# Kernel optimization log

Measured on AMD Instinct MI355X. Metric: run time of the kernel, lower is better.

## Reference

```python
import jax, jax.numpy as jnp
import numpy as np

D = 512          # feature dim
N = 4095         # context length
LMBD = 0.9       # eligibility-trace decay
DIM = 2 * D + 1  # 1025
CTX = N + 1      # 4096


def make_M(n: int, lmbd: float) -> jnp.ndarray:
    # M[row, col] = lmbd**(row-col) for col <= row < n, col < n; last row and
    # last column are all zero (M[-1, -1] explicitly zeroed in the original).
    i = jnp.arange(n, dtype=jnp.int32)
    diff = i[:, None] - i[None, :]
    core = jnp.where(diff >= 0, jnp.float32(lmbd) ** jnp.maximum(diff, 0).astype(jnp.float32), 0.0)
    M = jnp.zeros((n + 1, n + 1), dtype=jnp.float32)
    return M.at[:n, :n].set(core)


def setup_inputs() -> dict:
    key = jax.random.key(0)
    kz, kp, kq = jax.random.split(key, 3)
    Z = jax.random.normal(kz, (DIM, CTX), dtype=jnp.float32)
    # nn.Parameter(torch.empty(...)) is uninitialized in the source; use small
    # random values as stand-ins for trained parameters.
    P = jax.random.normal(kp, (DIM, DIM), dtype=jnp.float32) * 0.02
    Q = jax.random.normal(kq, (DIM, DIM), dtype=jnp.float32) * 0.02
    M = make_M(N, LMBD)
    return {"Z": Z, "P": P, "Q": Q, "M": M}


def reference(Z, P, Q, M):
    # X = Z^T Q Z : (CTX, CTX) bilinear attention scores
    X = jnp.einsum("dn,de,em->nm", Z, Q, Z)
    A = jax.nn.softmax(X, axis=-1)          # activation
    # Z + (1/n) * P @ Z @ M @ A ; contract left-to-right to keep (DIM, CTX) intermediates
    PZ = P @ Z                               # (DIM, CTX)
    PZM = PZ @ M                             # (DIM, CTX), M lower-tri decay
    return Z + (1.0 / N) * (PZM @ A)
```

## Files before the change

kernel.cpp:

```cpp
#include <hip/hip_runtime.h>


#define LMBD 0.9f
#define CTXN 4096
#define DIMN 1025
#define DP 1152

#define KSPLIT 1024
#define PSTRIDE ((size_t)DP * CTXN)

typedef __bf16 bf16x8 __attribute__((ext_vector_type(8)));
typedef float f32x4 __attribute__((ext_vector_type(4)));
typedef long lx2 __attribute__((ext_vector_type(2)));

__device__ __forceinline__ unsigned short f2bf(float f) {
  union { float f; unsigned u; } v; v.f = f;
  unsigned r = v.u + 0x7FFFu + ((v.u >> 16) & 1u);
  return (unsigned short)(r >> 16);
}
__device__ __forceinline__ float bf2f(unsigned short h) {
  union { unsigned u; float f; } v; v.u = ((unsigned)h) << 16;
  return v.f;
}

__device__ __forceinline__ void gld_lds16(const void* g, void* l) {
  __builtin_amdgcn_global_load_lds(
      (const __attribute__((address_space(1))) unsigned int*)g,
      (__attribute__((address_space(3))) unsigned int*)l, 16, 0, 0);
}

template <int MODE, int TM, int TN>
__device__ __forceinline__ void gemm_body(
    const unsigned short* __restrict__ A, const unsigned short* __restrict__ B,
    void* __restrict__ Cout, int K, int lda, int ldb, int ldc, int bi, int bj,
    float* __restrict__ pmax, float* __restrict__ psum) {
  constexpr int FI = TM / 32, FJ = TN / 32;
  __shared__ unsigned short sA[TM * 64];
  __shared__ unsigned short sB[TN * 64];
  const int tid = threadIdx.x;
  const int wave = tid >> 6;
  const int lane = tid & 63;
  const long i0 = (long)bi * TM;
  const long j0 = (long)bj * TN;
  const int wm = (wave & 1) * (TM / 2);
  const int wn = (wave >> 1) * (TN / 2);

  f32x4 acc[FI][FJ] = {};

  const int srow8 = lane >> 3;
  const int gk = ((lane & 7) - srow8) & 7;
  const int mrow = lane & 15;
  const int q2 = lane >> 4;

  for (int k0 = 0; k0 < K; k0 += 64) {
    __syncthreads();
#pragma unroll
    for (int c = 0; c < TM / 32; ++c) {
      const int q = wave * (TM / 32) + c;
      gld_lds16(A + (i0 + q * 8 + srow8) * (long)lda + k0 + gk * 8, &sA[q * 512]);
    }
#pragma unroll
    for (int c = 0; c < TN / 32; ++c) {
      const int q = wave * (TN / 32) + c;
      gld_lds16(B + (j0 + q * 8 + srow8) * (long)ldb + k0 + gk * 8, &sB[q * 512]);
    }
    __syncthreads();
#pragma unroll
    for (int kk = 0; kk < 2; ++kk) {
      const int slot = ((kk * 4 + q2) + mrow) & 7;
      bf16x8 af[FI], bfr[FJ];
#pragma unroll
      for (int i = 0; i < FI; ++i)
        af[i] = *(const bf16x8*)&sA[(wm + i * 16 + mrow) * 64 + slot * 8];
#pragma unroll
      for (int j = 0; j < FJ; ++j)
        bfr[j] = *(const bf16x8*)&sB[(wn + j * 16 + mrow) * 64 + slot * 8];
#pragma unroll
      for (int i = 0; i < FI; ++i)
#pragma unroll
        for (int j = 0; j < FJ; ++j)
          acc[i][j] =
              __builtin_amdgcn_mfma_f32_16x16x32_bf16(af[i], bfr[j], acc[i][j], 0, 0, 0);
    }
  }

  const int lr = (lane >> 4) * 4;
  const int lc = lane & 15;
#pragma unroll
  for (int i = 0; i < FI; ++i) {
#pragma unroll
    for (int j = 0; j < FJ; ++j) {
#pragma unroll
      for (int r = 0; r < 4; ++r) {
        const long row = i0 + wm + i * 16 + lr + r;
        const long col = j0 + wn + j * 16 + lc;
        const float v = acc[i][j][r];
        if (MODE == 1) ((float*)Cout)[row * ldc + col] = v;
        else ((unsigned short*)Cout)[row * ldc + col] = f2bf(v);
      }
    }
  }

  if constexpr (MODE == 4) {
    float* sMax = (float*)sA;
    float* sSum = (float*)sB;
    const int k8 = (wave & 1) * 4 + (lane >> 4);
    __syncthreads();
#pragma unroll
    for (int j = 0; j < FJ; ++j) {
      float m = -1e30f;
#pragma unroll
      for (int i = 0; i < FI; ++i)
#pragma unroll
        for (int r = 0; r < 4; ++r) m = fmaxf(m, acc[i][j][r]);
      float sv = 0.f;
#pragma unroll
      for (int i = 0; i < FI; ++i)
#pragma unroll
        for (int r = 0; r < 4; ++r) sv += __expf(acc[i][j][r] - m);
      const int c = wn + j * 16 + lc;
      sMax[c * 8 + k8] = m;
      sSum[c * 8 + k8] = sv;
    }
    __syncthreads();
    if (tid < 128) {
      float m = -1e30f;
#pragma unroll
      for (int k = 0; k < 8; ++k) m = fmaxf(m, sMax[tid * 8 + k]);
      float sv = 0.f;
#pragma unroll
      for (int k = 0; k < 8; ++k) sv += sSum[tid * 8 + k] * __expf(sMax[tid * 8 + k] - m);
      pmax[(size_t)bi * CTXN + j0 + tid] = m;
      psum[(size_t)bi * CTXN + j0 + tid] = sv;
    }
  }
}

__global__ __launch_bounds__(256, 2) void gemm_xt(
    const unsigned short* __restrict__ QZT, const unsigned short* __restrict__ ZbT,
    unsigned short* __restrict__ XT, float* __restrict__ pmax,
    float* __restrict__ psum) {
  gemm_body<4, 128, 128>(QZT, ZbT, XT, DP, DP, DP, CTXN, blockIdx.x, blockIdx.y, pmax,
                         psum);
}

__global__ __launch_bounds__(256, 2) void gemm_dual(
    const unsigned short* __restrict__ ZbT, const unsigned short* __restrict__ Qb,
    unsigned short* __restrict__ QZT, const unsigned short* __restrict__ Pb,
    float* __restrict__ PZ) {
  const unsigned g = blockIdx.x;
  if (g < 576) {
    gemm_body<0, 128, 64>(ZbT, Qb, QZT, DP, DP, DP, DP, g & 31, g >> 5, nullptr,
                          nullptr);
  } else {
    const unsigned h = g - 576;
    gemm_body<1, 64, 128>(Pb, ZbT, PZ, DP, DP, DP, CTXN, h >> 5, h & 31, nullptr,
                          nullptr);
  }
}

__global__ __launch_bounds__(256, 2) void gemm_fp8_splitk(
    const unsigned char* __restrict__ A, const unsigned char* __restrict__ B,
    unsigned short* __restrict__ Cout) {
  __shared__ unsigned char sA[128 * 64];
  __shared__ unsigned char sB[128 * 64];
  const int tid = threadIdx.x;
  const int wave = tid >> 6;
  const int lane = tid & 63;
  const unsigned g = blockIdx.x;
  const unsigned bj = g & 31;
  const unsigned t = g >> 5;
  const unsigned bi = t >> 2;
  const unsigned bz = t & 3;
  const long i0 = (long)bi * 128;
  const long j0 = (long)bj * 128;
  const int wm = (wave & 1) * 64;
  const int wn = (wave >> 1) * 64;
  const int kb = bz * KSPLIT;
  Cout += (size_t)bz * PSTRIDE;

  f32x4 acc[4][4] = {};
  const int srow = lane >> 2;
  const int skc = (((lane & 3) - (lane >> 3)) & 3) * 16;
  const int mrow = lane & 15;
  const int slot = ((((lane >> 4) + (mrow >> 1)) & 3)) * 16;

  for (int k0 = kb; k0 < kb + KSPLIT; k0 += 64) {
    __syncthreads();
#pragma unroll
    for (int c = 0; c < 2; ++c) {
      const int q = wave * 2 + c;
      gld_lds16(A + (i0 + q * 16 + srow) * (long)CTXN + k0 + skc, &sA[q * 1024]);
      gld_lds16(B + (j0 + q * 16 + srow) * (long)CTXN + k0 + skc, &sB[q * 1024]);
    }
    __syncthreads();
    lx2 af[4], bfr[4];
#pragma unroll
    for (int i = 0; i < 4; ++i)
      af[i] = *(const lx2*)&sA[(wm + i * 16 + mrow) * 64 + slot];
#pragma unroll
    for (int j = 0; j < 4; ++j)
      bfr[j] = *(const lx2*)&sB[(wn + j * 16 + mrow) * 64 + slot];
#pragma unroll
    for (int i = 0; i < 4; ++i)
#pragma unroll
      for (int j = 0; j < 4; ++j) {
        acc[i][j] = __builtin_amdgcn_mfma_f32_16x16x32_fp8_fp8(af[i].x, bfr[j].x,
                                                               acc[i][j], 0, 0, 0);
        acc[i][j] = __builtin_amdgcn_mfma_f32_16x16x32_fp8_fp8(af[i].y, bfr[j].y,
                                                               acc[i][j], 0, 0, 0);
      }
  }

  const int lr = (lane >> 4) * 4;
  const int lc = lane & 15;
#pragma unroll
  for (int i = 0; i < 4; ++i)
#pragma unroll
    for (int j = 0; j < 4; ++j)
#pragma unroll
      for (int r = 0; r < 4; ++r) {
        const long row = i0 + wm + i * 16 + lr + r;
        if (row < DIMN)
          Cout[row * (long)CTXN + j0 + wn + j * 16 + lc] = f2bf(acc[i][j][r]);
      }
}

__global__ void reduce_kernel(const unsigned short* __restrict__ Pt,
                              const float* __restrict__ Z, float* __restrict__ out) {
  const size_t idx = ((size_t)blockIdx.x * 256 + threadIdx.x) * 4;
  float ax = 0.f, ay = 0.f, az = 0.f, aw = 0.f;
#pragma unroll
  for (int z = 0; z < 4; ++z) {
    const ushort4 v = *(const ushort4*)&Pt[(size_t)z * PSTRIDE + idx];
    ax += bf2f(v.x); ay += bf2f(v.y); az += bf2f(v.z); aw += bf2f(v.w);
  }
  const f32x4 zv = *(const f32x4*)&Z[idx];
  f32x4 o;
  o[0] = zv[0] + ax * 0.00390625f;
  o[1] = zv[1] + ay * 0.00390625f;
  o[2] = zv[2] + az * 0.00390625f;
  o[3] = zv[3] + aw * 0.00390625f;
  *(f32x4*)&out[idx] = o;
}

__global__ void prep_kernel(const float* __restrict__ Z, const float* __restrict__ Q,
                            const float* __restrict__ P,
                            unsigned short* __restrict__ ZbT,
                            unsigned short* __restrict__ Qb,
                            unsigned short* __restrict__ Pb) {
  __shared__ float tile[32][33];
  const unsigned g = blockIdx.x;
  const int tid = threadIdx.x;
  if (g < 4608) {
    const int n0 = (g & 127) * 32, e0 = (g >> 7) * 32;
    const int tx = tid & 31, ty = tid >> 5;
#pragma unroll
    for (int k = 0; k < 4; ++k) {
      const int e = e0 + ty + k * 8;
      tile[ty + k * 8][tx] = (e < DIMN) ? Z[(size_t)e * CTXN + n0 + tx] : 0.f;
    }
    __syncthreads();
#pragma unroll
    for (int k = 0; k < 4; ++k) {
      const int n = n0 + ty + k * 8;
      ZbT[(size_t)n * DP + e0 + tx] = f2bf(tile[tx][ty + k * 8]);
    }
  } else {
    const unsigned id2 = g - 4608;
    const int mat = id2 >= 1296;
    const float* src = mat ? P : Q;
    unsigned short* dst = mat ? Pb : Qb;
    const unsigned e0 = (id2 - (mat ? 1296u : 0u)) * 1024u + tid * 4u;
    const unsigned r = e0 / 1152u;
    const unsigned c = e0 - r * 1152u;
    ushort4 o;
    o.x = (r < DIMN && c + 0 < DIMN) ? f2bf(src[(size_t)r * DIMN + c + 0]) : 0;
    o.y = (r < DIMN && c + 1 < DIMN) ? f2bf(src[(size_t)r * DIMN + c + 1]) : 0;
    o.z = (r < DIMN && c + 2 < DIMN) ? f2bf(src[(size_t)r * DIMN + c + 2]) : 0;
    o.w = (r < DIMN && c + 3 < DIMN) ? f2bf(src[(size_t)r * DIMN + c + 3]) : 0;
    *(ushort4*)&dst[(size_t)r * DP + c] = o;
  }
}

__global__ void red2_kernel(const float* __restrict__ pmax, const float* __restrict__ psum,
                            float* __restrict__ rowmax, float* __restrict__ inv_l) {
  const int n = blockIdx.x * 256 + threadIdx.x;
  float M = -1e30f;
  for (int c = 0; c < 32; ++c) M = fmaxf(M, pmax[(size_t)c * CTXN + n]);
  float s = 0.f;
  for (int c = 0; c < 32; ++c)
    s += psum[(size_t)c * CTXN + n] * __expf(pmax[(size_t)c * CTXN + n] - M);
  rowmax[n] = M;
  inv_l[n] = 1.0f / (4095.0f * s);
}

__global__ __launch_bounds__(256) void ewscan_kernel(
    const unsigned short* __restrict__ XT, const float* __restrict__ rowmax,
    unsigned int* __restrict__ ET, const float* __restrict__ PZ,
    const float* __restrict__ inv_l, unsigned char* __restrict__ PZMb) {
  __shared__ float sF[256];
  const unsigned g = blockIdx.x;
  const int t = threadIdx.x;
  if (g >= 1152) {
    const size_t idx = ((size_t)(g - 1152) * 256 + t) * 4;
    const ushort4 v = *(const ushort4*)&XT[idx];
    const int n = (int)(idx & 4095);
    const float4 rm = *(const float4*)&rowmax[n];
    unsigned p = __builtin_amdgcn_cvt_pk_fp8_f32(__expf(bf2f(v.x) - rm.x),
                                                 __expf(bf2f(v.y) - rm.y), 0, false);
    p = __builtin_amdgcn_cvt_pk_fp8_f32(__expf(bf2f(v.z) - rm.z),
                                        __expf(bf2f(v.w) - rm.w), p, true);
    ET[idx >> 2] = p;
    return;
  }
  const int d = g;
  const float* row = PZ + (size_t)d * CTXN;
  float x[16];
#pragma unroll
  for (int q = 0; q < 4; ++q) {
    const float4 v = *(const float4*)&row[t * 16 + q * 4];
    x[q * 4 + 0] = v.x; x[q * 4 + 1] = v.y; x[q * 4 + 2] = v.z; x[q * 4 + 3] = v.w;
  }
  if (t == 255) x[15] = 0.f;
  float loc[16];
  float run = 0.f;
#pragma unroll
  for (int i = 15; i >= 0; --i) { run = run * LMBD + x[i]; loc[i] = run; }
  float f = loc[0];
  sF[t] = f;
  __syncthreads();
  float mlt = 0.1853020188851841f;
  for (int step = 1; step < 256; step <<= 1) {
    const float other = (t + step < 256) ? sF[t + step] : 0.f;
    __syncthreads();
    f += mlt * other;
    mlt *= mlt;
    sF[t] = f;
    __syncthreads();
  }
  const float R = (t < 255) ? sF[t + 1] : 0.f;
  float il[16];
#pragma unroll
  for (int q = 0; q < 4; ++q) {
    const float4 v = *(const float4*)&inv_l[t * 16 + q * 4];
    il[q * 4 + 0] = v.x * 256.f; il[q * 4 + 1] = v.y * 256.f;
    il[q * 4 + 2] = v.z * 256.f; il[q * 4 + 3] = v.w * 256.f;
  }
  float o[16];
  float p = 1.f;
#pragma unroll
  for (int i = 15; i >= 0; --i) {
    p *= LMBD;
    o[i] = (loc[i] + p * R) * il[i];
  }
  unsigned w[4];
#pragma unroll
  for (int q = 0; q < 4; ++q) {
    unsigned pk = __builtin_amdgcn_cvt_pk_fp8_f32(o[q * 4 + 0], o[q * 4 + 1], 0, false);
    pk = __builtin_amdgcn_cvt_pk_fp8_f32(o[q * 4 + 2], o[q * 4 + 3], pk, true);
    w[q] = pk;
  }
  *(uint4*)&PZMb[(size_t)d * CTXN + t * 16] = make_uint4(w[0], w[1], w[2], w[3]);
}

extern "C" void kernel_launch(void* const* d_in, const int* in_sizes, int n_in,
                              void* d_out, int out_size, void* d_ws, size_t ws_size,
                              hipStream_t stream) {
  const float* Z = (const float*)d_in[0];
  const float* P = (const float*)d_in[1];
  const float* Q = (const float*)d_in[2];

  char* ws = (char*)d_ws;
  size_t off = 0;
  auto alloc = [&](size_t bytes) {
    void* p = ws + off;
    off += (bytes + 255) & ~(size_t)255;
    return p;
  };
  unsigned char* ET   = (unsigned char*)alloc((size_t)CTXN * CTXN);
  unsigned char* PZMb = (unsigned char*)alloc((size_t)DP * CTXN);
  float* rowmax       = (float*)alloc((size_t)CTXN * 4);
  float* inv_l        = (float*)alloc((size_t)CTXN * 4);
  char* pool = (char*)alloc(0);
  unsigned short* ZbT = (unsigned short*)alloc((size_t)CTXN * DP * 2);
  unsigned short* QZT = (unsigned short*)alloc((size_t)CTXN * DP * 2);
  unsigned short* XT  = (unsigned short*)alloc((size_t)CTXN * CTXN * 2);
  float* PZ           = (float*)alloc((size_t)DP * CTXN * 4);
  unsigned short* Qb  = (unsigned short*)alloc((size_t)DP * DP * 2);
  unsigned short* Pb  = (unsigned short*)alloc((size_t)DP * DP * 2);
  float* pmax         = (float*)alloc((size_t)32 * CTXN * 4);
  float* psum         = (float*)alloc((size_t)32 * CTXN * 4);
  unsigned short* partials = (unsigned short*)pool;
  if (off > ws_size) return;

  prep_kernel<<<7200, 256, 0, stream>>>(Z, Q, P, ZbT, Qb, Pb);

  gemm_dual<<<1152, 256, 0, stream>>>(ZbT, Qb, QZT, Pb, PZ);

  gemm_xt<<<dim3(32, 32), 256, 0, stream>>>(QZT, ZbT, XT, pmax, psum);

  red2_kernel<<<16, 256, 0, stream>>>(pmax, psum, rowmax, inv_l);

  ewscan_kernel<<<17536, 256, 0, stream>>>(XT, rowmax, (unsigned int*)ET, PZ, inv_l,
                                           PZMb);

  gemm_fp8_splitk<<<1152, 256, 0, stream>>>(PZMb, ET, partials);
  reduce_kernel<<<4100, 256, 0, stream>>>(partials, Z, (float*)d_out);
}
```

Measured before the change: 248.6 us.

## Fuse all stages into one cooperative persistent kernel with grid syncs

Replaces the seven separate kernel launches with a single cooperative kernel of 512 persistent blocks that loops over each stage's work units and separates stages with grid-wide syncs. Shared memory becomes one fixed 32KB buffer reused by every stage. The goal is to remove per-launch overhead and the tail gaps between kernels. In exchange, every stage runs at a fixed grid size and at the occupancy of the largest shared-memory user, and grid.sync adds its own cost. If the cooperative launch fails, the code falls back to the separate kernels.

```diff
diff --git a/kernel.cpp b/kernel.cpp
--- a/kernel.cpp
+++ b/kernel.cpp
@@ -1,4 +1,7 @@
 #include <hip/hip_runtime.h>
+#include <hip/hip_cooperative_groups.h>
+
+namespace cg = cooperative_groups;
 
 
 #define LMBD 0.9f
@@ -13,6 +16,15 @@
 typedef float f32x4 __attribute__((ext_vector_type(4)));
 typedef long lx2 __attribute__((ext_vector_type(2)));
 
+struct KParams {
+  const float *Z, *P, *Q;
+  unsigned short *ZbT, *QZT, *XT, *Qb, *Pb;
+  float *PZ, *pmax, *psum, *rowmax, *inv_l;
+  unsigned char *ET, *PZMb;
+  unsigned short *partials;
+  float *out;
+};
+
 __device__ __forceinline__ unsigned short f2bf(float f) {
   union { float f; unsigned u; } v; v.f = f;
   unsigned r = v.u + 0x7FFFu + ((v.u >> 16) & 1u);
@@ -31,12 +43,13 @@
 
 template <int MODE, int TM, int TN>
 __device__ __forceinline__ void gemm_body(
-    const unsigned short* __restrict__ A, const unsigned short* __restrict__ B,
-    void* __restrict__ Cout, int K, int lda, int ldb, int ldc, int bi, int bj,
-    float* __restrict__ pmax, float* __restrict__ psum) {
+    char* smem, const unsigned short* __restrict__ A,
+    const unsigned short* __restrict__ B, void* __restrict__ Cout, int K, int lda,
+    int ldb, int ldc, int bi, int bj, float* __restrict__ pmax,
+    float* __restrict__ psum) {
   constexpr int FI = TM / 32, FJ = TN / 32;
-  __shared__ unsigned short sA[TM * 64];
-  __shared__ unsigned short sB[TN * 64];
+  unsigned short* sA = (unsigned short*)smem;
+  unsigned short* sB = sA + TM * 64;
   const int tid = threadIdx.x;
   const int wave = tid >> 6;
   const int lane = tid & 63;
@@ -136,38 +149,140 @@
   }
 }
 
-__global__ __launch_bounds__(256, 2) void gemm_xt(
-    const unsigned short* __restrict__ QZT, const unsigned short* __restrict__ ZbT,
-    unsigned short* __restrict__ XT, float* __restrict__ pmax,
-    float* __restrict__ psum) {
-  gemm_body<4, 128, 128>(QZT, ZbT, XT, DP, DP, DP, CTXN, blockIdx.x, blockIdx.y, pmax,
-                         psum);
-}
-
-__global__ __launch_bounds__(256, 2) void gemm_dual(
-    const unsigned short* __restrict__ ZbT, const unsigned short* __restrict__ Qb,
-    unsigned short* __restrict__ QZT, const unsigned short* __restrict__ Pb,
-    float* __restrict__ PZ) {
-  const unsigned g = blockIdx.x;
+
+__device__ __forceinline__ void prep_unit(char* smem, unsigned g, const KParams& a) {
+  float* tile = (float*)smem;
+  const int tid = threadIdx.x;
+  if (g < 4608) {
+    const int n0 = (g & 127) * 32, e0 = (g >> 7) * 32;
+    const int tx = tid & 31, ty = tid >> 5;
+    __syncthreads();
+#pragma unroll
+    for (int k = 0; k < 4; ++k) {
+      const int e = e0 + ty + k * 8;
+      tile[(ty + k * 8) * 33 + tx] = (e < DIMN) ? a.Z[(size_t)e * CTXN + n0 + tx] : 0.f;
+    }
+    __syncthreads();
+#pragma unroll
+    for (int k = 0; k < 4; ++k) {
+      const int n = n0 + ty + k * 8;
+      a.ZbT[(size_t)n * DP + e0 + tx] = f2bf(tile[tx * 33 + ty + k * 8]);
+    }
+  } else {
+    const unsigned id2 = g - 4608;
+    const int mat = id2 >= 1296;
+    const float* src = mat ? a.P : a.Q;
+    unsigned short* dst = mat ? a.Pb : a.Qb;
+    const unsigned e0 = (id2 - (mat ? 1296u : 0u)) * 1024u + tid * 4u;
+    const unsigned r = e0 / 1152u;
+    const unsigned c = e0 - r * 1152u;
+    ushort4 o;
+    o.x = (r < DIMN && c + 0 < DIMN) ? f2bf(src[(size_t)r * DIMN + c + 0]) : 0;
+    o.y = (r < DIMN && c + 1 < DIMN) ? f2bf(src[(size_t)r * DIMN + c + 1]) : 0;
+    o.z = (r < DIMN && c + 2 < DIMN) ? f2bf(src[(size_t)r * DIMN + c + 2]) : 0;
+    o.w = (r < DIMN && c + 3 < DIMN) ? f2bf(src[(size_t)r * DIMN + c + 3]) : 0;
+    *(ushort4*)&dst[(size_t)r * DP + c] = o;
+  }
+}
+
+__device__ __forceinline__ void dual_unit(char* smem, unsigned g, const KParams& a) {
   if (g < 576) {
-    gemm_body<0, 128, 64>(ZbT, Qb, QZT, DP, DP, DP, DP, g & 31, g >> 5, nullptr,
-                          nullptr);
+    gemm_body<0, 128, 64>(smem, a.ZbT, a.Qb, a.QZT, DP, DP, DP, DP, g & 31, g >> 5,
+                          nullptr, nullptr);
   } else {
     const unsigned h = g - 576;
-    gemm_body<1, 64, 128>(Pb, ZbT, PZ, DP, DP, DP, CTXN, h >> 5, h & 31, nullptr,
-                          nullptr);
-  }
-}
-
-__global__ __launch_bounds__(256, 2) void gemm_fp8_splitk(
-    const unsigned char* __restrict__ A, const unsigned char* __restrict__ B,
-    unsigned short* __restrict__ Cout) {
-  __shared__ unsigned char sA[128 * 64];
-  __shared__ unsigned char sB[128 * 64];
+    gemm_body<1, 64, 128>(smem, a.Pb, a.ZbT, a.PZ, DP, DP, DP, CTXN, h >> 5, h & 31,
+                          nullptr, nullptr);
+  }
+}
+
+__device__ __forceinline__ void xt_unit(char* smem, unsigned u, const KParams& a) {
+  gemm_body<4, 128, 128>(smem, a.QZT, a.ZbT, a.XT, DP, DP, DP, CTXN, u & 31, u >> 5,
+                         a.pmax, a.psum);
+}
+
+__device__ __forceinline__ void red2_unit(unsigned u, const KParams& a) {
+  const int n = (int)u * 256 + threadIdx.x;
+  float M = -1e30f;
+  for (int c = 0; c < 32; ++c) M = fmaxf(M, a.pmax[(size_t)c * CTXN + n]);
+  float s = 0.f;
+  for (int c = 0; c < 32; ++c)
+    s += a.psum[(size_t)c * CTXN + n] * __expf(a.pmax[(size_t)c * CTXN + n] - M);
+  a.rowmax[n] = M;
+  a.inv_l[n] = 1.0f / (4095.0f * s);
+}
+
+__device__ __forceinline__ void ewscan_unit(float* sF, unsigned g, const KParams& a) {
+  const int t = threadIdx.x;
+  if (g >= 1152) {
+    const size_t idx = ((size_t)(g - 1152) * 256 + t) * 4;
+    const ushort4 v = *(const ushort4*)&a.XT[idx];
+    const int n = (int)(idx & 4095);
+    const float4 rm = *(const float4*)&a.rowmax[n];
+    unsigned p = __builtin_amdgcn_cvt_pk_fp8_f32(__expf(bf2f(v.x) - rm.x),
+                                                 __expf(bf2f(v.y) - rm.y), 0, false);
+    p = __builtin_amdgcn_cvt_pk_fp8_f32(__expf(bf2f(v.z) - rm.z),
+                                        __expf(bf2f(v.w) - rm.w), p, true);
+    ((unsigned int*)a.ET)[idx >> 2] = p;
+    return;
+  }
+  const int d = (int)g;
+  const float* row = a.PZ + (size_t)d * CTXN;
+  float x[16];
+#pragma unroll
+  for (int q = 0; q < 4; ++q) {
+    const float4 v = *(const float4*)&row[t * 16 + q * 4];
+    x[q * 4 + 0] = v.x; x[q * 4 + 1] = v.y; x[q * 4 + 2] = v.z; x[q * 4 + 3] = v.w;
+  }
+  if (t == 255) x[15] = 0.f;
+  float loc[16];
+  float run = 0.f;
+#pragma unroll
+  for (int i = 15; i >= 0; --i) { run = run * LMBD + x[i]; loc[i] = run; }
+  __syncthreads();
+  float f = loc[0];
+  sF[t] = f;
+  __syncthreads();
+  float mlt = 0.1853020188851841f;
+  for (int step = 1; step < 256; step <<= 1) {
+    const float other = (t + step < 256) ? sF[t + step] : 0.f;
+    __syncthreads();
+    f += mlt * other;
+    mlt *= mlt;
+    sF[t] = f;
+    __syncthreads();
+  }
+  const float R = (t < 255) ? sF[t + 1] : 0.f;
+  float il[16];
+#pragma unroll
+  for (int q = 0; q < 4; ++q) {
+    const float4 v = *(const float4*)&a.inv_l[t * 16 + q * 4];
+    il[q * 4 + 0] = v.x * 256.f; il[q * 4 + 1] = v.y * 256.f;
+    il[q * 4 + 2] = v.z * 256.f; il[q * 4 + 3] = v.w * 256.f;
+  }
+  float o[16];
+  float p = 1.f;
+#pragma unroll
+  for (int i = 15; i >= 0; --i) {
+    p *= LMBD;
+    o[i] = (loc[i] + p * R) * il[i];
+  }
+  unsigned w[4];
+#pragma unroll
+  for (int q = 0; q < 4; ++q) {
+    unsigned pk = __builtin_amdgcn_cvt_pk_fp8_f32(o[q * 4 + 0], o[q * 4 + 1], 0, false);
+    pk = __builtin_amdgcn_cvt_pk_fp8_f32(o[q * 4 + 2], o[q * 4 + 3], pk, true);
+    w[q] = pk;
+  }
+  *(uint4*)&a.PZMb[(size_t)d * CTXN + t * 16] = make_uint4(w[0], w[1], w[2], w[3]);
+}
+
+__device__ __forceinline__ void fp8_unit(char* smem, unsigned g, const KParams& a) {
+  unsigned char* sA = (unsigned char*)smem;
+  unsigned char* sB = sA + 128 * 64;
   const int tid = threadIdx.x;
   const int wave = tid >> 6;
   const int lane = tid & 63;
-  const unsigned g = blockIdx.x;
   const unsigned bj = g & 31;
   const unsigned t = g >> 5;
   const unsigned bi = t >> 2;
@@ -177,7 +292,7 @@
   const int wm = (wave & 1) * 64;
   const int wn = (wave >> 1) * 64;
   const int kb = bz * KSPLIT;
-  Cout += (size_t)bz * PSTRIDE;
+  unsigned short* Cout = a.partials + (size_t)bz * PSTRIDE;
 
   f32x4 acc[4][4] = {};
   const int srow = lane >> 2;
@@ -190,8 +305,8 @@
 #pragma unroll
     for (int c = 0; c < 2; ++c) {
       const int q = wave * 2 + c;
-      gld_lds16(A + (i0 + q * 16 + srow) * (long)CTXN + k0 + skc, &sA[q * 1024]);
-      gld_lds16(B + (j0 + q * 16 + srow) * (long)CTXN + k0 + skc, &sB[q * 1024]);
+      gld_lds16(a.PZMb + (i0 + q * 16 + srow) * (long)CTXN + k0 + skc, &sA[q * 1024]);
+      gld_lds16(a.ET + (j0 + q * 16 + srow) * (long)CTXN + k0 + skc, &sB[q * 1024]);
     }
     __syncthreads();
     lx2 af[4], bfr[4];
@@ -226,150 +341,74 @@
       }
 }
 
-__global__ void reduce_kernel(const unsigned short* __restrict__ Pt,
-                              const float* __restrict__ Z, float* __restrict__ out) {
-  const size_t idx = ((size_t)blockIdx.x * 256 + threadIdx.x) * 4;
+__device__ __forceinline__ void reduce_unit(unsigned u, const KParams& a) {
+  const size_t idx = ((size_t)u * 256 + threadIdx.x) * 4;
   float ax = 0.f, ay = 0.f, az = 0.f, aw = 0.f;
 #pragma unroll
   for (int z = 0; z < 4; ++z) {
-    const ushort4 v = *(const ushort4*)&Pt[(size_t)z * PSTRIDE + idx];
+    const ushort4 v = *(const ushort4*)&a.partials[(size_t)z * PSTRIDE + idx];
     ax += bf2f(v.x); ay += bf2f(v.y); az += bf2f(v.z); aw += bf2f(v.w);
   }
-  const f32x4 zv = *(const f32x4*)&Z[idx];
+  const f32x4 zv = *(const f32x4*)&a.Z[idx];
   f32x4 o;
   o[0] = zv[0] + ax * 0.00390625f;
   o[1] = zv[1] + ay * 0.00390625f;
   o[2] = zv[2] + az * 0.00390625f;
   o[3] = zv[3] + aw * 0.00390625f;
-  *(f32x4*)&out[idx] = o;
-}
-
-__global__ void prep_kernel(const float* __restrict__ Z, const float* __restrict__ Q,
-                            const float* __restrict__ P,
-                            unsigned short* __restrict__ ZbT,
-                            unsigned short* __restrict__ Qb,
-                            unsigned short* __restrict__ Pb) {
-  __shared__ float tile[32][33];
-  const unsigned g = blockIdx.x;
-  const int tid = threadIdx.x;
-  if (g < 4608) {
-    const int n0 = (g & 127) * 32, e0 = (g >> 7) * 32;
-    const int tx = tid & 31, ty = tid >> 5;
-#pragma unroll
-    for (int k = 0; k < 4; ++k) {
-      const int e = e0 + ty + k * 8;
-      tile[ty + k * 8][tx] = (e < DIMN) ? Z[(size_t)e * CTXN + n0 + tx] : 0.f;
-    }
-    __syncthreads();
-#pragma unroll
-    for (int k = 0; k < 4; ++k) {
-      const int n = n0 + ty + k * 8;
-      ZbT[(size_t)n * DP + e0 + tx] = f2bf(tile[tx][ty + k * 8]);
-    }
-  } else {
-    const unsigned id2 = g - 4608;
-    const int mat = id2 >= 1296;
-    const float* src = mat ? P : Q;
-    unsigned short* dst = mat ? Pb : Qb;
-    const unsigned e0 = (id2 - (mat ? 1296u : 0u)) * 1024u + tid * 4u;
-    const unsigned r = e0 / 1152u;
-    const unsigned c = e0 - r * 1152u;
-    ushort4 o;
-    o.x = (r < DIMN && c + 0 < DIMN) ? f2bf(src[(size_t)r * DIMN + c + 0]) : 0;
-    o.y = (r < DIMN && c + 1 < DIMN) ? f2bf(src[(size_t)r * DIMN + c + 1]) : 0;
-    o.z = (r < DIMN && c + 2 < DIMN) ? f2bf(src[(size_t)r * DIMN + c + 2]) : 0;
-    o.w = (r < DIMN && c + 3 < DIMN) ? f2bf(src[(size_t)r * DIMN + c + 3]) : 0;
-    *(ushort4*)&dst[(size_t)r * DP + c] = o;
-  }
-}
-
-__global__ void red2_kernel(const float* __restrict__ pmax, const float* __restrict__ psum,
-                            float* __restrict__ rowmax, float* __restrict__ inv_l) {
-  const int n = blockIdx.x * 256 + threadIdx.x;
-  float M = -1e30f;
-  for (int c = 0; c < 32; ++c) M = fmaxf(M, pmax[(size_t)c * CTXN + n]);
-  float s = 0.f;
-  for (int c = 0; c < 32; ++c)
-    s += psum[(size_t)c * CTXN + n] * __expf(pmax[(size_t)c * CTXN + n] - M);
-  rowmax[n] = M;
-  inv_l[n] = 1.0f / (4095.0f * s);
-}
-
-__global__ __launch_bounds__(256) void ewscan_kernel(
-    const unsigned short* __restrict__ XT, const float* __restrict__ rowmax,
-    unsigned int* __restrict__ ET, const float* __restrict__ PZ,
-    const float* __restrict__ inv_l, unsigned char* __restrict__ PZMb) {
+  *(f32x4*)&a.out[idx] = o;
+}
+
+__global__ __launch_bounds__(256, 2) void mega(KParams a) {
+  __shared__ __align__(16) char smem[32768];
+  cg::grid_group grid = cg::this_grid();
+  const unsigned nb = gridDim.x;
+  const unsigned b0 = blockIdx.x;
+
+  for (unsigned u = b0; u < 7200; u += nb) prep_unit(smem, u, a);
+  grid.sync();
+  for (unsigned u = b0; u < 1152; u += nb) dual_unit(smem, u, a);
+  grid.sync();
+  for (unsigned u = b0; u < 1024; u += nb) xt_unit(smem, u, a);
+  grid.sync();
+  for (unsigned u = b0; u < 16; u += nb) red2_unit(u, a);
+  grid.sync();
+  for (unsigned u = b0; u < 17536; u += nb) ewscan_unit((float*)smem, u, a);
+  grid.sync();
+  for (unsigned u = b0; u < 1152; u += nb) fp8_unit(smem, u, a);
+  grid.sync();
+  for (unsigned u = b0; u < 4100; u += nb) reduce_unit(u, a);
+}
+
+__global__ void prep_k(KParams a) {
+  __shared__ __align__(16) char smem[4352];
+  prep_unit(smem, blockIdx.x, a);
+}
+__global__ __launch_bounds__(256, 2) void dual_k(KParams a) {
+  __shared__ __align__(16) char smem[24576];
+  dual_unit(smem, blockIdx.x, a);
+}
+__global__ __launch_bounds__(256, 2) void xt_k(KParams a) {
+  __shared__ __align__(16) char smem[32768];
+  xt_unit(smem, blockIdx.x, a);
+}
+__global__ void red2_k(KParams a) { red2_unit(blockIdx.x, a); }
+__global__ __launch_bounds__(256) void ewscan_k(KParams a) {
   __shared__ float sF[256];
-  const unsigned g = blockIdx.x;
-  const int t = threadIdx.x;
-  if (g >= 1152) {
-    const size_t idx = ((size_t)(g - 1152) * 256 + t) * 4;
-    const ushort4 v = *(const ushort4*)&XT[idx];
-    const int n = (int)(idx & 4095);
-    const float4 rm = *(const float4*)&rowmax[n];
-    unsigned p = __builtin_amdgcn_cvt_pk_fp8_f32(__expf(bf2f(v.x) - rm.x),
-                                                 __expf(bf2f(v.y) - rm.y), 0, false);
-    p = __builtin_amdgcn_cvt_pk_fp8_f32(__expf(bf2f(v.z) - rm.z),
-                                        __expf(bf2f(v.w) - rm.w), p, true);
-    ET[idx >> 2] = p;
-    return;
-  }
-  const int d = g;
-  const float* row = PZ + (size_t)d * CTXN;
-  float x[16];
-#pragma unroll
-  for (int q = 0; q < 4; ++q) {
-    const float4 v = *(const float4*)&row[t * 16 + q * 4];
-    x[q * 4 + 0] = v.x; x[q * 4 + 1] = v.y; x[q * 4 + 2] = v.z; x[q * 4 + 3] = v.w;
-  }
-  if (t == 255) x[15] = 0.f;
-  float loc[16];
-  float run = 0.f;
-#pragma unroll
-  for (int i = 15; i >= 0; --i) { run = run * LMBD + x[i]; loc[i] = run; }
-  float f = loc[0];
-  sF[t] = f;
-  __syncthreads();
-  float mlt = 0.1853020188851841f;
-  for (int step = 1; step < 256; step <<= 1) {
-    const float other = (t + step < 256) ? sF[t + step] : 0.f;
-    __syncthreads();
-    f += mlt * other;
-    mlt *= mlt;
-    sF[t] = f;
-    __syncthreads();
-  }
-  const float R = (t < 255) ? sF[t + 1] : 0.f;
-  float il[16];
-#pragma unroll
-  for (int q = 0; q < 4; ++q) {
-    const float4 v = *(const float4*)&inv_l[t * 16 + q * 4];
-    il[q * 4 + 0] = v.x * 256.f; il[q * 4 + 1] = v.y * 256.f;
-    il[q * 4 + 2] = v.z * 256.f; il[q * 4 + 3] = v.w * 256.f;
-  }
-  float o[16];
-  float p = 1.f;
-#pragma unroll
-  for (int i = 15; i >= 0; --i) {
-    p *= LMBD;
-    o[i] = (loc[i] + p * R) * il[i];
-  }
-  unsigned w[4];
-#pragma unroll
-  for (int q = 0; q < 4; ++q) {
-    unsigned pk = __builtin_amdgcn_cvt_pk_fp8_f32(o[q * 4 + 0], o[q * 4 + 1], 0, false);
-    pk = __builtin_amdgcn_cvt_pk_fp8_f32(o[q * 4 + 2], o[q * 4 + 3], pk, true);
-    w[q] = pk;
-  }
-  *(uint4*)&PZMb[(size_t)d * CTXN + t * 16] = make_uint4(w[0], w[1], w[2], w[3]);
-}
+  ewscan_unit(sF, blockIdx.x, a);
+}
+__global__ __launch_bounds__(256, 2) void fp8_k(KParams a) {
+  __shared__ __align__(16) char smem[16384];
+  fp8_unit(smem, blockIdx.x, a);
+}
+__global__ void reduce_k(KParams a) { reduce_unit(blockIdx.x, a); }
 
 extern "C" void kernel_launch(void* const* d_in, const int* in_sizes, int n_in,
                               void* d_out, int out_size, void* d_ws, size_t ws_size,
                               hipStream_t stream) {
-  const float* Z = (const float*)d_in[0];
-  const float* P = (const float*)d_in[1];
-  const float* Q = (const float*)d_in[2];
+  KParams a;
+  a.Z = (const float*)d_in[0];
+  a.P = (const float*)d_in[1];
+  a.Q = (const float*)d_in[2];
 
   char* ws = (char*)d_ws;
   size_t off = 0;
@@ -378,33 +417,34 @@
     off += (bytes + 255) & ~(size_t)255;
     return p;
   };
-  unsigned char* ET   = (unsigned char*)alloc((size_t)CTXN * CTXN);
-  unsigned char* PZMb = (unsigned char*)alloc((size_t)DP * CTXN);
-  float* rowmax       = (float*)alloc((size_t)CTXN * 4);
-  float* inv_l        = (float*)alloc((size_t)CTXN * 4);
+  a.ET     = (unsigned char*)alloc((size_t)CTXN * CTXN);
+  a.PZMb   = (unsigned char*)alloc((size_t)DP * CTXN);
+  a.rowmax = (float*)alloc((size_t)CTXN * 4);
+  a.inv_l  = (float*)alloc((size_t)CTXN * 4);
   char* pool = (char*)alloc(0);
-  unsigned short* ZbT = (unsigned short*)alloc((size_t)CTXN * DP * 2);
-  unsigned short* QZT = (unsigned short*)alloc((size_t)CTXN * DP * 2);
-  unsigned short* XT  = (unsigned short*)alloc((size_t)CTXN * CTXN * 2);
-  float* PZ           = (float*)alloc((size_t)DP * CTXN * 4);
-  unsigned short* Qb  = (unsigned short*)alloc((size_t)DP * DP * 2);
-  unsigned short* Pb  = (unsigned short*)alloc((size_t)DP * DP * 2);
-  float* pmax         = (float*)alloc((size_t)32 * CTXN * 4);
-  float* psum         = (float*)alloc((size_t)32 * CTXN * 4);
-  unsigned short* partials = (unsigned short*)pool;
+  a.ZbT  = (unsigned short*)alloc((size_t)CTXN * DP * 2);
+  a.QZT  = (unsigned short*)alloc((size_t)CTXN * DP * 2);
+  a.XT   = (unsigned short*)alloc((size_t)CTXN * CTXN * 2);
+  a.PZ   = (float*)alloc((size_t)DP * CTXN * 4);
+  a.Qb   = (unsigned short*)alloc((size_t)DP * DP * 2);
+  a.Pb   = (unsigned short*)alloc((size_t)DP * DP * 2);
+  a.pmax = (float*)alloc((size_t)32 * CTXN * 4);
+  a.psum = (float*)alloc((size_t)32 * CTXN * 4);
+  a.partials = (unsigned short*)pool;
+  a.out = (float*)d_out;
   if (off > ws_size) return;
 
-  prep_kernel<<<7200, 256, 0, stream>>>(Z, Q, P, ZbT, Qb, Pb);
-
-  gemm_dual<<<1152, 256, 0, stream>>>(ZbT, Qb, QZT, Pb, PZ);
-
-  gemm_xt<<<dim3(32, 32), 256, 0, stream>>>(QZT, ZbT, XT, pmax, psum);
-
-  red2_kernel<<<16, 256, 0, stream>>>(pmax, psum, rowmax, inv_l);
-
-  ewscan_kernel<<<17536, 256, 0, stream>>>(XT, rowmax, (unsigned int*)ET, PZ, inv_l,
-                                           PZMb);
-
-  gemm_fp8_splitk<<<1152, 256, 0, stream>>>(PZMb, ET, partials);
-  reduce_kernel<<<4100, 256, 0, stream>>>(partials, Z, (float*)d_out);
-}
+  void* kargs[] = {(void*)&a};
+  hipError_t err =
+      hipLaunchCooperativeKernel(mega, dim3(512), dim3(256), kargs, 0u, stream);
+  if (err != hipSuccess) {
+    (void)hipGetLastError();
+    prep_k<<<7200, 256, 0, stream>>>(a);
+    dual_k<<<1152, 256, 0, stream>>>(a);
+    xt_k<<<1024, 256, 0, stream>>>(a);
+    red2_k<<<16, 256, 0, stream>>>(a);
+    ewscan_k<<<17536, 256, 0, stream>>>(a);
+    fp8_k<<<1152, 256, 0, stream>>>(a);
+    reduce_k<<<4100, 256, 0, stream>>>(a);
+  }
+}
```

Measured after the change: 665.3 us. 168% more time.
